# Kernel tuning notes

Measured on AMD Instinct MI355X. Metric: run time of the kernel, lower is better.

Reference implementation:

```python
import jax, jax.numpy as jnp
import numpy as np

NEG_SLOPE = 0.2
BN_EPS = 1e-5


def setup_inputs() -> dict:
    key = jax.random.key(0)
    ks = jax.random.split(key, 12)
    N, E, F_IN, H, C, G, LAT = 50000, 1600000, 128, 2, 64, 512, 32
    x = jax.random.normal(ks[0], (N, F_IN), dtype=jnp.float32)
    edge_index = jax.random.randint(ks[1], (2, E), 0, N, dtype=jnp.int64)
    batch = jnp.sort(jax.random.randint(ks[2], (N,), 0, G, dtype=jnp.int64))
    # GATConv params (PyG layout): lin is Linear(F_IN, H*C, bias=False)
    lin_w = jax.random.normal(ks[3], (H * C, F_IN), dtype=jnp.float32) / np.sqrt(F_IN)
    att_src = jax.random.normal(ks[4], (1, H, C), dtype=jnp.float32) / np.sqrt(C)
    att_dst = jax.random.normal(ks[5], (1, H, C), dtype=jnp.float32) / np.sqrt(C)
    bias = jnp.zeros((H * C,), dtype=jnp.float32)
    bn_gamma = jnp.ones((H * C,), dtype=jnp.float32)
    bn_beta = jnp.zeros((H * C,), dtype=jnp.float32)
    fc_w = jax.random.normal(ks[6], (LAT, H * C), dtype=jnp.float32) / np.sqrt(H * C)
    fc_b = jnp.zeros((LAT,), dtype=jnp.float32)
    return {"x": x, "edge_index": edge_index, "batch": batch, "num_graphs": G,
            "lin_w": lin_w, "att_src": att_src, "att_dst": att_dst, "bias": bias,
            "bn_gamma": bn_gamma, "bn_beta": bn_beta, "fc_w": fc_w, "fc_b": fc_b}


def _gat_conv(x, src, dst, lin_w, att_src, att_dst, bias):
    N = x.shape[0]
    H, C = att_src.shape[1], att_src.shape[2]
    h = (x @ lin_w.T).reshape(N, H, C)                     # [N,H,C]
    a_src = (h * att_src).sum(-1)                          # [N,H]
    a_dst = (h * att_dst).sum(-1)                          # [N,H]
    e = a_src[src] + a_dst[dst]                            # [E,H]
    e = jnp.where(e > 0, e, NEG_SLOPE * e)                 # leaky_relu(0.2)
    # segment softmax over incoming edges of each dst node
    m = jax.ops.segment_max(e, dst, num_segments=N)        # [N,H]
    p = jnp.exp(e - m[dst])
    s = jax.ops.segment_sum(p, dst, num_segments=N)        # [N,H]
    alpha = p / s[dst]                                     # [E,H]
    msg = h[src] * alpha[:, :, None]                       # [E,H,C]
    out = jax.ops.segment_sum(msg, dst, num_segments=N)    # [N,H,C]
    return out.reshape(N, H * C) + bias


def reference(x, edge_index, batch, num_graphs, lin_w, att_src, att_dst, bias,
              bn_gamma, bn_beta, fc_w, fc_b):
    N = x.shape[0]
    loops = jnp.arange(N, dtype=edge_index.dtype)
    src = jnp.concatenate([edge_index[0], loops])          # add_self_loops=True
    dst = jnp.concatenate([edge_index[1], loops])
    h = _gat_conv(x, src, dst, lin_w, att_src, att_dst, bias)
    pooled = jax.ops.segment_sum(h, batch, num_segments=num_graphs)  # [G, H*C]
    mu = pooled.mean(0)
    var = pooled.var(0)
    out = (pooled - mu) / jnp.sqrt(var + BN_EPS) * bn_gamma + bn_beta
    return out @ fc_w.T + fc_b
```

## Files before the change

kernel.cpp:

```cpp
#include <hip/hip_runtime.h>
#include <hip/hip_bf16.h>


#define BKT_SHIFT 8
#define BKT_MASK  255
#define BKT_CAP   14336
#define BIN_TILE  4096

typedef __attribute__((ext_vector_type(8))) short bf16x8;
typedef __attribute__((ext_vector_type(4))) float f32x4;

static __device__ __forceinline__ float lo16(unsigned int u) {
    union { unsigned int i; float f; } c; c.i = u << 16; return c.f;
}
static __device__ __forceinline__ float hi16(unsigned int u) {
    union { unsigned int i; float f; } c; c.i = u & 0xffff0000u; return c.f;
}
static __device__ __forceinline__ unsigned short f2bf(float f) {
    unsigned int b = __builtin_bit_cast(unsigned int, f);
    return (unsigned short)((b >> 16) + ((b >> 15) & 1));
}
static __device__ __forceinline__ float rlane_f(float x, int l) {
    return __builtin_bit_cast(float, __builtin_amdgcn_readlane(__builtin_bit_cast(int, x), l));
}

__global__ __launch_bounds__(256) void k_histprep(const int* __restrict__ ei, int E,
                                                  int* __restrict__ blkhist, int NB,
                                                  const float* __restrict__ w,
                                                  unsigned short* __restrict__ wb,
                                                  float* __restrict__ pooled,
                                                  long long npool, int nbin) {
    const int t = threadIdx.x;
    const int bid = blockIdx.x;
    if (bid < nbin) {
        __shared__ int cnt[1024];
        for (int i = t; i < 1024; i += 256) cnt[i] = 0;
        __syncthreads();
        int base = bid * BIN_TILE;
        int end = min(base + BIN_TILE, E);
        for (int i = base + t; i < end; i += 256)
            atomicAdd(&cnt[ei[E + i] >> BKT_SHIFT], 1);
        __syncthreads();
        int* row = blkhist + (size_t)bid * NB;
        for (int b = t; b < NB; b += 256) row[b] = cnt[b];
    } else if (bid < nbin + 64) {
        int i = (bid - nbin) * 256 + t;
        wb[i] = f2bf(w[i]);
    } else {
        long long i = (long long)(bid - nbin - 64) * 256 + t;
        for (; i < npool; i += 64 * 256) pooled[i] = 0.f;
    }
}

__global__ __launch_bounds__(256) void k_linscan(const float* __restrict__ x,
                                                 const unsigned short* __restrict__ wb,
                                                 const float* __restrict__ att_s,
                                                 const float* __restrict__ att_d,
                                                 unsigned short* __restrict__ h2,
                                                 float* __restrict__ asrc,
                                                 float* __restrict__ adst, int N,
                                                 int* __restrict__ blkhist,
                                                 int* __restrict__ tot,
                                                 int NB, int nbin, int nlin) {
    const int t = threadIdx.x;
    if ((int)blockIdx.x >= nlin) {
        int b = (blockIdx.x - nlin) * 4 + (t >> 6);
        int lane = t & 63;
        if (b >= NB) return;
        int run = 0;
        for (int blk0 = 0; blk0 < nbin; blk0 += 64) {
            int idx = blk0 + lane;
            int v = (idx < nbin) ? blkhist[(size_t)idx * NB + b] : 0;
            int inc = v;
#pragma unroll
            for (int off = 1; off < 64; off <<= 1) {
                int u = __shfl_up(inc, off);
                if (lane >= off) inc += u;
            }
            if (idx < nbin) blkhist[(size_t)idx * NB + b] = run + (inc - v);
            run += __shfl(inc, 63);
        }
        if (lane == 0) tot[b] = run;
        return;
    }
    const int lane = t & 63;
    const int wid = t >> 6;
    const int row0 = (blockIdx.x * 4 + wid) * 16;
    const int rlo = lane & 15;
    const int khi = lane >> 4;

    int arow = row0 + rlo; if (arow >= N) arow = N - 1;
    const float* xrow = x + (long long)arow * 128;
    bf16x8 afrag[4];
#pragma unroll
    for (int ks = 0; ks < 4; ++ks) {
        int k0 = ks * 32 + khi * 8;
        float4 xa = *(const float4*)(xrow + k0);
        float4 xb = *(const float4*)(xrow + k0 + 4);
        bf16x8 a;
        a[0] = (short)f2bf(xa.x); a[1] = (short)f2bf(xa.y);
        a[2] = (short)f2bf(xa.z); a[3] = (short)f2bf(xa.w);
        a[4] = (short)f2bf(xb.x); a[5] = (short)f2bf(xb.y);
        a[6] = (short)f2bf(xb.z); a[7] = (short)f2bf(xb.w);
        afrag[ks] = a;
    }

    float ps0[4] = {0.f,0.f,0.f,0.f}, pd0[4] = {0.f,0.f,0.f,0.f};
    float ps1[4] = {0.f,0.f,0.f,0.f}, pd1[4] = {0.f,0.f,0.f,0.f};

    for (int ct = 0; ct < 8; ++ct) {
        const int col = ct * 16 + rlo;
        f32x4 acc = {0.f, 0.f, 0.f, 0.f};
#pragma unroll
        for (int ks = 0; ks < 4; ++ks) {
            bf16x8 b = *(const bf16x8*)(wb + (size_t)col * 128 + ks * 32 + khi * 8);
            acc = __builtin_amdgcn_mfma_f32_16x16x32_bf16(afrag[ks], b, acc, 0, 0, 0);
        }
        const float as = att_s[col], ad = att_d[col];
        const bool head0 = (ct < 4);
#pragma unroll
        for (int r = 0; r < 4; ++r) {
            int row = row0 + khi * 4 + r;
            if (row < N) h2[(long long)row * 128 + col] = f2bf(acc[r]);
            float v = acc[r];
            if (head0) { ps0[r] = fmaf(v, as, ps0[r]); pd0[r] = fmaf(v, ad, pd0[r]); }
            else       { ps1[r] = fmaf(v, as, ps1[r]); pd1[r] = fmaf(v, ad, pd1[r]); }
        }
    }

#pragma unroll
    for (int off = 1; off <= 8; off <<= 1) {
#pragma unroll
        for (int r = 0; r < 4; ++r) {
            ps0[r] += __shfl_xor(ps0[r], off);
            pd0[r] += __shfl_xor(pd0[r], off);
            ps1[r] += __shfl_xor(ps1[r], off);
            pd1[r] += __shfl_xor(pd1[r], off);
        }
    }
    if (rlo == 0) {
#pragma unroll
        for (int r = 0; r < 4; ++r) {
            int row = row0 + khi * 4 + r;
            if (row < N) {
                asrc[row * 2]     = ps0[r];
                asrc[row * 2 + 1] = ps1[r];
                adst[row * 2]     = pd0[r];
                adst[row * 2 + 1] = pd1[r];
            }
        }
    }
}

__global__ __launch_bounds__(256) void k_bin(const int* __restrict__ ei, int E,
                                             const int* __restrict__ blkhist,
                                             const int* __restrict__ tot,
                                             unsigned int* __restrict__ stage, int NB) {
    __shared__ int gb[1024];
    __shared__ int cnt[1024];
    __shared__ int part[256];
    int t = threadIdx.x;
    const int* row = blkhist + (size_t)blockIdx.x * NB;
    int vals[4]; int s0 = 0;
#pragma unroll
    for (int k = 0; k < 4; ++k) {
        int b2 = t * 4 + k;
        vals[k] = (b2 < NB) ? tot[b2] : 0;
        s0 += vals[k];
    }
    part[t] = s0;
    __syncthreads();
    for (int off = 1; off < 256; off <<= 1) {
        int u = (t >= off) ? part[t - off] : 0;
        __syncthreads();
        part[t] += u;
        __syncthreads();
    }
    int base = part[t] - s0;
#pragma unroll
    for (int k = 0; k < 4; ++k) {
        int b2 = t * 4 + k;
        if (b2 < NB) { gb[b2] = base + row[b2]; cnt[b2] = 0; }
        base += vals[k];
    }
    __syncthreads();
    int ebase = blockIdx.x * BIN_TILE;
    int eend = min(ebase + BIN_TILE, E);
    for (int i = ebase + t; i < eend; i += 256) {
        int s = ei[i];
        int d = ei[E + i];
        int b = d >> BKT_SHIFT;
        int off = atomicAdd(&cnt[b], 1);
        stage[gb[b] + off] = ((unsigned int)(d & BKT_MASK) << 24) | (unsigned int)s;
    }
}

__global__ __launch_bounds__(256) void k_bsort(const int* __restrict__ tot,
                                               const unsigned int* __restrict__ stage,
                                               int* __restrict__ rowptr,
                                               int* __restrict__ csr,
                                               int N, int E, int NB) {
    __shared__ int hist[256];
    __shared__ int sc[256];
    __shared__ int rp[256];
    __shared__ int lc[256];
    __shared__ int part[256];
    __shared__ int s_bb, s_be;
    __shared__ int lout[BKT_CAP];
    int b = blockIdx.x;
    int node0 = b << BKT_SHIFT;
    int nloc = min(256, N - node0);
    int t = threadIdx.x;

    int vals[4]; int s0 = 0;
#pragma unroll
    for (int k = 0; k < 4; ++k) {
        int b2 = t * 4 + k;
        vals[k] = (b2 < NB) ? tot[b2] : 0;
        s0 += vals[k];
    }
    part[t] = s0;
    __syncthreads();
    for (int off = 1; off < 256; off <<= 1) {
        int u = (t >= off) ? part[t - off] : 0;
        __syncthreads();
        part[t] += u;
        __syncthreads();
    }
    int base = part[t] - s0;
#pragma unroll
    for (int k = 0; k < 4; ++k) {
        int b2 = t * 4 + k;
        if (b2 == b) { s_bb = base; s_be = base + vals[k]; }
        base += vals[k];
    }
    __syncthreads();
    const int bb = s_bb, be = s_be;

    hist[t] = 0; lc[t] = 0;
    __syncthreads();
    for (int i = bb + t; i < be; i += 256)
        atomicAdd(&hist[stage[i] >> 24], 1);
    __syncthreads();
    sc[t] = hist[t];
    __syncthreads();
    for (int off = 1; off < 256; off <<= 1) {
        int u = (t >= off) ? sc[t - off] : 0;
        __syncthreads();
        sc[t] += u;
        __syncthreads();
    }
    int rpg = bb + sc[t] - hist[t];
    rp[t] = rpg;
    if (t < nloc) rowptr[node0 + t] = rpg;
    if (b == 0 && t == 0) rowptr[N] = E;
    __syncthreads();
    for (int i = bb + t; i < be; i += 256) {
        unsigned int wrec = stage[i];
        int dl = (int)(wrec >> 24);
        int src = (int)(wrec & 0x00FFFFFFu);
        int pos = rp[dl] + atomicAdd(&lc[dl], 1);
        int rel = pos - bb;
        if (rel < BKT_CAP) lout[rel] = src;
        else csr[pos] = src;
    }
    __syncthreads();
    int cntb = be - bb; if (cntb > BKT_CAP) cntb = BKT_CAP;
    for (int i = t; i < cntb; i += 256) csr[bb + i] = lout[i];
}

__global__ __launch_bounds__(256) void k_agg(const int* __restrict__ rowptr,
                                             const int* __restrict__ csr_src,
                                             const unsigned short* __restrict__ h2,
                                             const float* __restrict__ asrc,
                                             const float* __restrict__ adst,
                                             const float* __restrict__ bias,
                                             const int* __restrict__ batch,
                                             float* __restrict__ pooled, int N) {
    int n = __builtin_amdgcn_readfirstlane(blockIdx.x * 4 + (threadIdx.x >> 6));
    const int lane = threadIdx.x & 63;
    if (n >= N) return;
    const bool lo = (lane < 32);
    const int el = lane & 31;

    float2 adn = *(const float2*)(adst + (size_t)n * 2);
    float2 asn = *(const float2*)(asrc + (size_t)n * 2);
    float e0 = asn.x + adn.x; e0 = e0 > 0.f ? e0 : 0.2f * e0;
    float e1 = asn.y + adn.y; e1 = e1 > 0.f ? e1 : 0.2f * e1;
    float w0 = __expf(e0), w1 = __expf(e1);

    unsigned int v = ((const unsigned int*)(h2 + (size_t)n * 128))[lane];
    float wh = lo ? w0 : w1;
    float aX = wh * lo16(v), aY = wh * hi16(v);
    float ps = 0.f;
    const float adh = lo ? adn.x : adn.y;

    const int beg = rowptr[n], end = rowptr[n + 1];
    for (int base = beg; base < end; base += 32) {
        int cnt = min(32, end - base);
        int sv = n;
        if (el < cnt) sv = csr_src[base + el];
        float av = asrc[(size_t)sv * 2 + (lo ? 0 : 1)];
        float f = av + adh; f = f > 0.f ? f : 0.2f * f;
        float usel = (el < cnt) ? __expf(f) : 0.f;
        ps += usel;

        int k = 0;
        for (; k + 8 <= cnt; k += 8) {
#pragma unroll
            for (int j = 0; j < 8; ++j) {
                int e = k + j;
                int se = __builtin_amdgcn_readlane(sv, e);
                float su0 = rlane_f(usel, e);
                float su1 = rlane_f(usel, e + 32);
                float uu = lo ? su0 : su1;
                unsigned int vv = ((const unsigned int*)(h2 + (size_t)se * 128))[lane];
                aX = fmaf(uu, lo16(vv), aX);
                aY = fmaf(uu, hi16(vv), aY);
            }
        }
        for (; k < cnt; ++k) {
            int se = __builtin_amdgcn_readlane(sv, k);
            float su0 = rlane_f(usel, k);
            float su1 = rlane_f(usel, k + 32);
            float uu = lo ? su0 : su1;
            unsigned int vv = ((const unsigned int*)(h2 + (size_t)se * 128))[lane];
            aX = fmaf(uu, lo16(vv), aX);
            aY = fmaf(uu, hi16(vv), aY);
        }
    }

#pragma unroll
    for (int off = 1; off <= 16; off <<= 1)
        ps += __shfl_xor(ps, off);
    float sdiv = ps + (lo ? w0 : w1);

    int j0 = lane * 2;
    float2 bv = *(const float2*)(bias + j0);
    float o0 = aX / sdiv + bv.x;
    float o1 = aY / sdiv + bv.y;
    int g = batch[n];
    atomicAdd(&pooled[(size_t)g * 128 + j0], o0);
    atomicAdd(&pooled[(size_t)g * 128 + j0 + 1], o1);
}

__global__ __launch_bounds__(512) void k_bnstat(const float* __restrict__ pooled,
                                                const float* __restrict__ gamma,
                                                const float* __restrict__ beta,
                                                float* __restrict__ scale,
                                                float* __restrict__ shift, int G) {
    __shared__ float ls[512], lq[512];
    int t = threadIdx.x;
    int j = t & 127, q = t >> 7;
    int per = G >> 2;
    float sum = 0.f, sq = 0.f;
    for (int g = q * per; g < (q + 1) * per; ++g) {
        float v = pooled[g * 128 + j];
        sum += v; sq += v * v;
    }
    ls[t] = sum; lq[t] = sq;
    __syncthreads();
    if (t < 128) {
        sum = ls[t] + ls[t + 128] + ls[t + 256] + ls[t + 384];
        sq  = lq[t] + lq[t + 128] + lq[t + 256] + lq[t + 384];
        float mu = sum / (float)G;
        float var = sq / (float)G - mu * mu;
        float sc = gamma[t] * rsqrtf(var + 1e-5f);
        scale[t] = sc;
        shift[t] = beta[t] - mu * sc;
    }
}

__global__ __launch_bounds__(128) void k_fc(const float* __restrict__ pooled,
                                            const float* __restrict__ scale,
                                            const float* __restrict__ shift,
                                            const float* __restrict__ fcw,
                                            const float* __restrict__ fcb,
                                            float* __restrict__ out, int LAT) {
    __shared__ float nrm[128];
    int g = blockIdx.x;
    int t = threadIdx.x;
    nrm[t] = pooled[g * 128 + t] * scale[t] + shift[t];
    __syncthreads();
    if (t < LAT) {
        float acc = fcb[t];
#pragma unroll 8
        for (int j = 0; j < 128; ++j)
            acc = fmaf(nrm[j], fcw[t * 128 + j], acc);
        out[g * LAT + t] = acc;
    }
}

extern "C" void kernel_launch(void* const* d_in, const int* in_sizes, int n_in,
                              void* d_out, int out_size, void* d_ws, size_t ws_size,
                              hipStream_t stream) {
    const float* x     = (const float*)d_in[0];
    const int*   ei    = (const int*)d_in[1];
    const int*   batch = (const int*)d_in[2];
    const float* lin_w = (const float*)d_in[4];
    const float* att_s = (const float*)d_in[5];
    const float* att_d = (const float*)d_in[6];
    const float* bias  = (const float*)d_in[7];
    const float* gamma = (const float*)d_in[8];
    const float* beta  = (const float*)d_in[9];
    const float* fcw   = (const float*)d_in[10];
    const float* fcb   = (const float*)d_in[11];
    float* out = (float*)d_out;

    const int N   = in_sizes[2];
    const int E   = in_sizes[1] / 2;
    const int LAT = in_sizes[11];
    const int G   = out_size / LAT;
    const int NB  = (N + 255) >> BKT_SHIFT;
    const int nbin = (E + BIN_TILE - 1) / BIN_TILE;
    const int nlin = (N + 63) / 64;

    char* ws = (char*)d_ws;
    unsigned short* h2 = (unsigned short*)ws; ws += (size_t)N * 128 * 2;
    unsigned short* wb = (unsigned short*)ws; ws += (size_t)128 * 128 * 2;
    float* asrc   = (float*)ws; ws += (size_t)N * 2 * 4;
    float* adst   = (float*)ws; ws += (size_t)N * 2 * 4;
    float* pooled = (float*)ws; ws += (size_t)G * 128 * 4;
    float* scale  = (float*)ws; ws += 128 * 4;
    float* shift  = (float*)ws; ws += 128 * 4;
    int*   tot    = (int*)ws;   ws += (size_t)NB * 4;
    int*   blkhist= (int*)ws;   ws += (size_t)nbin * NB * 4;
    int*   rowptr = (int*)ws;   ws += (size_t)(N + 1) * 4;
    unsigned int* stage = (unsigned int*)ws; ws += (size_t)E * 4;
    int*   csr    = (int*)ws;   ws += (size_t)E * 4;

    k_histprep<<<nbin + 128, 256, 0, stream>>>(ei, E, blkhist, NB, lin_w, wb,
                                               pooled, (long long)G * 128, nbin);
    k_linscan<<<nlin + (NB + 3) / 4, 256, 0, stream>>>(x, wb, att_s, att_d, h2,
                                                       asrc, adst, N, blkhist, tot,
                                                       NB, nbin, nlin);
    k_bin<<<nbin, 256, 0, stream>>>(ei, E, blkhist, tot, stage, NB);
    k_bsort<<<NB, 256, 0, stream>>>(tot, stage, rowptr, csr, N, E, NB);
    k_agg<<<(N + 3) / 4, 256, 0, stream>>>(rowptr, csr, h2, asrc, adst, bias, batch, pooled, N);
    k_bnstat<<<1, 512, 0, stream>>>(pooled, gamma, beta, scale, shift, G);
    k_fc<<<G, 128, 0, stream>>>(pooled, scale, shift, fcw, fcb, out, LAT);
}
```

Before: 179.6 us.

## Fuse CSR build phases into one cooperative kernel and merge BN stats into FC

The histogram, per-bucket scan, edge binning and bucket sort now run as phases of one persistent cooperative kernel separated by grid-wide syncs, instead of four separate launches. The linear projection moves into its own kernel. Batch-norm statistics are recomputed inside each FC block, which removes the single-block stats kernel and the scale/shift buffers. This cuts launch gaps and serialization between small kernels. In exchange it adds grid-sync cost, duplicates the stats reduction across all G blocks, and no longer overlaps the projection with the scan.

After: 327.5 us. +82.4%, slower.

```diff
diff --git a/kernel.cpp b/kernel.cpp
--- a/kernel.cpp
+++ b/kernel.cpp
@@ -1,5 +1,8 @@
 #include <hip/hip_runtime.h>
 #include <hip/hip_bf16.h>
+#include <hip/hip_cooperative_groups.h>
+
+namespace cg = cooperative_groups;
 
 
 #define BKT_SHIFT 8
@@ -24,65 +27,186 @@
     return __builtin_bit_cast(float, __builtin_amdgcn_readlane(__builtin_bit_cast(int, x), l));
 }
 
-__global__ __launch_bounds__(256) void k_histprep(const int* __restrict__ ei, int E,
-                                                  int* __restrict__ blkhist, int NB,
-                                                  const float* __restrict__ w,
-                                                  unsigned short* __restrict__ wb,
-                                                  float* __restrict__ pooled,
-                                                  long long npool, int nbin) {
+__global__ __launch_bounds__(256) void k_csr(const int* __restrict__ ei, int E,
+                                             int* __restrict__ blkhist, int NB,
+                                             const float* __restrict__ w,
+                                             unsigned short* __restrict__ wb,
+                                             float* __restrict__ pooled,
+                                             long long npool, int nbin,
+                                             int* __restrict__ tot,
+                                             int* __restrict__ rowptr,
+                                             int* __restrict__ csr,
+                                             unsigned int* __restrict__ stage,
+                                             int N) {
+    __shared__ int smem[15618];
+    cg::grid_group grid = cg::this_grid();
     const int t = threadIdx.x;
-    const int bid = blockIdx.x;
-    if (bid < nbin) {
-        __shared__ int cnt[1024];
-        for (int i = t; i < 1024; i += 256) cnt[i] = 0;
-        __syncthreads();
-        int base = bid * BIN_TILE;
-        int end = min(base + BIN_TILE, E);
-        for (int i = base + t; i < end; i += 256)
-            atomicAdd(&cnt[ei[E + i] >> BKT_SHIFT], 1);
-        __syncthreads();
-        int* row = blkhist + (size_t)bid * NB;
-        for (int b = t; b < NB; b += 256) row[b] = cnt[b];
-    } else if (bid < nbin + 64) {
-        int i = (bid - nbin) * 256 + t;
-        wb[i] = f2bf(w[i]);
-    } else {
-        long long i = (long long)(bid - nbin - 64) * 256 + t;
-        for (; i < npool; i += 64 * 256) pooled[i] = 0.f;
-    }
-}
-
-__global__ __launch_bounds__(256) void k_linscan(const float* __restrict__ x,
-                                                 const unsigned short* __restrict__ wb,
-                                                 const float* __restrict__ att_s,
-                                                 const float* __restrict__ att_d,
-                                                 unsigned short* __restrict__ h2,
-                                                 float* __restrict__ asrc,
-                                                 float* __restrict__ adst, int N,
-                                                 int* __restrict__ blkhist,
-                                                 int* __restrict__ tot,
-                                                 int NB, int nbin, int nlin) {
+    const int nblk = gridDim.x;
+
+    for (int vb = blockIdx.x; vb < nbin + 128; vb += nblk) {
+        if (vb < nbin) {
+            int* cnt = smem;
+            for (int i = t; i < 1024; i += 256) cnt[i] = 0;
+            __syncthreads();
+            int base = vb * BIN_TILE;
+            int end = min(base + BIN_TILE, E);
+            for (int i = base + t; i < end; i += 256)
+                atomicAdd(&cnt[ei[E + i] >> BKT_SHIFT], 1);
+            __syncthreads();
+            int* row = blkhist + (size_t)vb * NB;
+            for (int b = t; b < NB; b += 256) row[b] = cnt[b];
+            __syncthreads();
+        } else if (vb < nbin + 64) {
+            int i = (vb - nbin) * 256 + t;
+            wb[i] = f2bf(w[i]);
+        } else {
+            long long i = (long long)(vb - nbin - 64) * 256 + t;
+            for (; i < npool; i += 64 * 256) pooled[i] = 0.f;
+        }
+    }
+    grid.sync();
+
+    for (int vb = blockIdx.x; vb < (NB + 3) / 4; vb += nblk) {
+        int b = vb * 4 + (t >> 6);
+        int lane = t & 63;
+        if (b < NB) {
+            int run = 0;
+            for (int blk0 = 0; blk0 < nbin; blk0 += 64) {
+                int idx = blk0 + lane;
+                int v = (idx < nbin) ? blkhist[(size_t)idx * NB + b] : 0;
+                int inc = v;
+#pragma unroll
+                for (int off = 1; off < 64; off <<= 1) {
+                    int u = __shfl_up(inc, off);
+                    if (lane >= off) inc += u;
+                }
+                if (idx < nbin) blkhist[(size_t)idx * NB + b] = run + (inc - v);
+                run += __shfl(inc, 63);
+            }
+            if (lane == 0) tot[b] = run;
+        }
+    }
+    grid.sync();
+
+    for (int vb = blockIdx.x; vb < nbin; vb += nblk) {
+        int* gb   = smem;
+        int* cnt  = smem + 1024;
+        int* part = smem + 2048;
+        const int* row = blkhist + (size_t)vb * NB;
+        int vals[4]; int s0 = 0;
+#pragma unroll
+        for (int k = 0; k < 4; ++k) {
+            int b2 = t * 4 + k;
+            vals[k] = (b2 < NB) ? tot[b2] : 0;
+            s0 += vals[k];
+        }
+        part[t] = s0;
+        __syncthreads();
+        for (int off = 1; off < 256; off <<= 1) {
+            int u = (t >= off) ? part[t - off] : 0;
+            __syncthreads();
+            part[t] += u;
+            __syncthreads();
+        }
+        int base = part[t] - s0;
+#pragma unroll
+        for (int k = 0; k < 4; ++k) {
+            int b2 = t * 4 + k;
+            if (b2 < NB) { gb[b2] = base + row[b2]; cnt[b2] = 0; }
+            base += vals[k];
+        }
+        __syncthreads();
+        int ebase = vb * BIN_TILE;
+        int eend = min(ebase + BIN_TILE, E);
+        for (int i = ebase + t; i < eend; i += 256) {
+            int s = ei[i];
+            int d = ei[E + i];
+            int b = d >> BKT_SHIFT;
+            int off = atomicAdd(&cnt[b], 1);
+            stage[gb[b] + off] = ((unsigned int)(d & BKT_MASK) << 24) | (unsigned int)s;
+        }
+        __syncthreads();
+    }
+    grid.sync();
+
+    for (int vb = blockIdx.x; vb < NB; vb += nblk) {
+        int* lout = smem;
+        int* hist = smem + 14336;
+        int* sc   = smem + 14592;
+        int* rp   = smem + 14848;
+        int* lc   = smem + 15104;
+        int* part = smem + 15360;
+        int* sbb  = smem + 15616;
+        int node0 = vb << BKT_SHIFT;
+        int nloc = min(256, N - node0);
+
+        int vals[4]; int s0 = 0;
+#pragma unroll
+        for (int k = 0; k < 4; ++k) {
+            int b2 = t * 4 + k;
+            vals[k] = (b2 < NB) ? tot[b2] : 0;
+            s0 += vals[k];
+        }
+        part[t] = s0;
+        __syncthreads();
+        for (int off = 1; off < 256; off <<= 1) {
+            int u = (t >= off) ? part[t - off] : 0;
+            __syncthreads();
+            part[t] += u;
+            __syncthreads();
+        }
+        int base = part[t] - s0;
+#pragma unroll
+        for (int k = 0; k < 4; ++k) {
+            int b2 = t * 4 + k;
+            if (b2 == vb) { sbb[0] = base; sbb[1] = base + vals[k]; }
+            base += vals[k];
+        }
+        __syncthreads();
+        const int bb = sbb[0], be = sbb[1];
+
+        hist[t] = 0; lc[t] = 0;
+        __syncthreads();
+        for (int i = bb + t; i < be; i += 256)
+            atomicAdd(&hist[stage[i] >> 24], 1);
+        __syncthreads();
+        sc[t] = hist[t];
+        __syncthreads();
+        for (int off = 1; off < 256; off <<= 1) {
+            int u = (t >= off) ? sc[t - off] : 0;
+            __syncthreads();
+            sc[t] += u;
+            __syncthreads();
+        }
+        int rpg = bb + sc[t] - hist[t];
+        rp[t] = rpg;
+        if (t < nloc) rowptr[node0 + t] = rpg;
+        if (vb == 0 && t == 0) rowptr[N] = E;
+        __syncthreads();
+        for (int i = bb + t; i < be; i += 256) {
+            unsigned int wrec = stage[i];
+            int dl = (int)(wrec >> 24);
+            int src = (int)(wrec & 0x00FFFFFFu);
+            int pos = rp[dl] + atomicAdd(&lc[dl], 1);
+            int rel = pos - bb;
+            if (rel < BKT_CAP) lout[rel] = src;
+            else csr[pos] = src;
+        }
+        __syncthreads();
+        int cntb = be - bb; if (cntb > BKT_CAP) cntb = BKT_CAP;
+        for (int i = t; i < cntb; i += 256) csr[bb + i] = lout[i];
+        __syncthreads();
+    }
+}
+
+__global__ __launch_bounds__(256) void k_lin(const float* __restrict__ x,
+                                             const unsigned short* __restrict__ wb,
+                                             const float* __restrict__ att_s,
+                                             const float* __restrict__ att_d,
+                                             unsigned short* __restrict__ h2,
+                                             float* __restrict__ asrc,
+                                             float* __restrict__ adst, int N) {
     const int t = threadIdx.x;
-    if ((int)blockIdx.x >= nlin) {
-        int b = (blockIdx.x - nlin) * 4 + (t >> 6);
-        int lane = t & 63;
-        if (b >= NB) return;
-        int run = 0;
-        for (int blk0 = 0; blk0 < nbin; blk0 += 64) {
-            int idx = blk0 + lane;
-            int v = (idx < nbin) ? blkhist[(size_t)idx * NB + b] : 0;
-            int inc = v;
-#pragma unroll
-            for (int off = 1; off < 64; off <<= 1) {
-                int u = __shfl_up(inc, off);
-                if (lane >= off) inc += u;
-            }
-            if (idx < nbin) blkhist[(size_t)idx * NB + b] = run + (inc - v);
-            run += __shfl(inc, 63);
-        }
-        if (lane == 0) tot[b] = run;
-        return;
-    }
     const int lane = t & 63;
     const int wid = t >> 6;
     const int row0 = (blockIdx.x * 4 + wid) * 16;
@@ -150,123 +274,6 @@
             }
         }
     }
-}
-
-__global__ __launch_bounds__(256) void k_bin(const int* __restrict__ ei, int E,
-                                             const int* __restrict__ blkhist,
-                                             const int* __restrict__ tot,
-                                             unsigned int* __restrict__ stage, int NB) {
-    __shared__ int gb[1024];
-    __shared__ int cnt[1024];
-    __shared__ int part[256];
-    int t = threadIdx.x;
-    const int* row = blkhist + (size_t)blockIdx.x * NB;
-    int vals[4]; int s0 = 0;
-#pragma unroll
-    for (int k = 0; k < 4; ++k) {
-        int b2 = t * 4 + k;
-        vals[k] = (b2 < NB) ? tot[b2] : 0;
-        s0 += vals[k];
-    }
-    part[t] = s0;
-    __syncthreads();
-    for (int off = 1; off < 256; off <<= 1) {
-        int u = (t >= off) ? part[t - off] : 0;
-        __syncthreads();
-        part[t] += u;
-        __syncthreads();
-    }
-    int base = part[t] - s0;
-#pragma unroll
-    for (int k = 0; k < 4; ++k) {
-        int b2 = t * 4 + k;
-        if (b2 < NB) { gb[b2] = base + row[b2]; cnt[b2] = 0; }
-        base += vals[k];
-    }
-    __syncthreads();
-    int ebase = blockIdx.x * BIN_TILE;
-    int eend = min(ebase + BIN_TILE, E);
-    for (int i = ebase + t; i < eend; i += 256) {
-        int s = ei[i];
-        int d = ei[E + i];
-        int b = d >> BKT_SHIFT;
-        int off = atomicAdd(&cnt[b], 1);
-        stage[gb[b] + off] = ((unsigned int)(d & BKT_MASK) << 24) | (unsigned int)s;
-    }
-}
-
-__global__ __launch_bounds__(256) void k_bsort(const int* __restrict__ tot,
-                                               const unsigned int* __restrict__ stage,
-                                               int* __restrict__ rowptr,
-                                               int* __restrict__ csr,
-                                               int N, int E, int NB) {
-    __shared__ int hist[256];
-    __shared__ int sc[256];
-    __shared__ int rp[256];
-    __shared__ int lc[256];
-    __shared__ int part[256];
-    __shared__ int s_bb, s_be;
-    __shared__ int lout[BKT_CAP];
-    int b = blockIdx.x;
-    int node0 = b << BKT_SHIFT;
-    int nloc = min(256, N - node0);
-    int t = threadIdx.x;
-
-    int vals[4]; int s0 = 0;
-#pragma unroll
-    for (int k = 0; k < 4; ++k) {
-        int b2 = t * 4 + k;
-        vals[k] = (b2 < NB) ? tot[b2] : 0;
-        s0 += vals[k];
-    }
-    part[t] = s0;
-    __syncthreads();
-    for (int off = 1; off < 256; off <<= 1) {
-        int u = (t >= off) ? part[t - off] : 0;
-        __syncthreads();
-        part[t] += u;
-        __syncthreads();
-    }
-    int base = part[t] - s0;
-#pragma unroll
-    for (int k = 0; k < 4; ++k) {
-        int b2 = t * 4 + k;
-        if (b2 == b) { s_bb = base; s_be = base + vals[k]; }
-        base += vals[k];
-    }
-    __syncthreads();
-    const int bb = s_bb, be = s_be;
-
-    hist[t] = 0; lc[t] = 0;
-    __syncthreads();
-    for (int i = bb + t; i < be; i += 256)
-        atomicAdd(&hist[stage[i] >> 24], 1);
-    __syncthreads();
-    sc[t] = hist[t];
-    __syncthreads();
-    for (int off = 1; off < 256; off <<= 1) {
-        int u = (t >= off) ? sc[t - off] : 0;
-        __syncthreads();
-        sc[t] += u;
-        __syncthreads();
-    }
-    int rpg = bb + sc[t] - hist[t];
-    rp[t] = rpg;
-    if (t < nloc) rowptr[node0 + t] = rpg;
-    if (b == 0 && t == 0) rowptr[N] = E;
-    __syncthreads();
-    for (int i = bb + t; i < be; i += 256) {
-        unsigned int wrec = stage[i];
-        int dl = (int)(wrec >> 24);
-        int src = (int)(wrec & 0x00FFFFFFu);
-        int pos = rp[dl] + atomicAdd(&lc[dl], 1);
-        int rel = pos - bb;
-        if (rel < BKT_CAP) lout[rel] = src;
-        else csr[pos] = src;
-    }
-    __syncthreads();
-    int cntb = be - bb; if (cntb > BKT_CAP) cntb = BKT_CAP;
-    for (int i = t; i < cntb; i += 256) csr[bb + i] = lout[i];
 }
 
 __global__ __launch_bounds__(256) void k_agg(const int* __restrict__ rowptr,
@@ -344,43 +351,27 @@
     atomicAdd(&pooled[(size_t)g * 128 + j0 + 1], o1);
 }
 
-__global__ __launch_bounds__(512) void k_bnstat(const float* __restrict__ pooled,
+__global__ __launch_bounds__(128) void k_fcstat(const float* __restrict__ pooled,
                                                 const float* __restrict__ gamma,
                                                 const float* __restrict__ beta,
-                                                float* __restrict__ scale,
-                                                float* __restrict__ shift, int G) {
-    __shared__ float ls[512], lq[512];
+                                                const float* __restrict__ fcw,
+                                                const float* __restrict__ fcb,
+                                                float* __restrict__ out, int G, int LAT) {
+    __shared__ float nrm[128];
     int t = threadIdx.x;
-    int j = t & 127, q = t >> 7;
-    int per = G >> 2;
     float sum = 0.f, sq = 0.f;
-    for (int g = q * per; g < (q + 1) * per; ++g) {
-        float v = pooled[g * 128 + j];
+#pragma unroll 8
+    for (int g = 0; g < G; ++g) {
+        float v = pooled[(size_t)g * 128 + t];
         sum += v; sq += v * v;
     }
-    ls[t] = sum; lq[t] = sq;
-    __syncthreads();
-    if (t < 128) {
-        sum = ls[t] + ls[t + 128] + ls[t + 256] + ls[t + 384];
-        sq  = lq[t] + lq[t + 128] + lq[t + 256] + lq[t + 384];
-        float mu = sum / (float)G;
-        float var = sq / (float)G - mu * mu;
-        float sc = gamma[t] * rsqrtf(var + 1e-5f);
-        scale[t] = sc;
-        shift[t] = beta[t] - mu * sc;
-    }
-}
-
-__global__ __launch_bounds__(128) void k_fc(const float* __restrict__ pooled,
-                                            const float* __restrict__ scale,
-                                            const float* __restrict__ shift,
-                                            const float* __restrict__ fcw,
-                                            const float* __restrict__ fcb,
-                                            float* __restrict__ out, int LAT) {
-    __shared__ float nrm[128];
+    float mu = sum / (float)G;
+    float var = sq / (float)G - mu * mu;
+    float sc = gamma[t] * rsqrtf(var + 1e-5f);
+    float sh = beta[t] - mu * sc;
+
     int g = blockIdx.x;
-    int t = threadIdx.x;
-    nrm[t] = pooled[g * 128 + t] * scale[t] + shift[t];
+    nrm[t] = pooled[(size_t)g * 128 + t] * sc + sh;
     __syncthreads();
     if (t < LAT) {
         float acc = fcb[t];
@@ -421,22 +412,24 @@
     float* asrc   = (float*)ws; ws += (size_t)N * 2 * 4;
     float* adst   = (float*)ws; ws += (size_t)N * 2 * 4;
     float* pooled = (float*)ws; ws += (size_t)G * 128 * 4;
-    float* scale  = (float*)ws; ws += 128 * 4;
-    float* shift  = (float*)ws; ws += 128 * 4;
     int*   tot    = (int*)ws;   ws += (size_t)NB * 4;
     int*   blkhist= (int*)ws;   ws += (size_t)nbin * NB * 4;
     int*   rowptr = (int*)ws;   ws += (size_t)(N + 1) * 4;
     unsigned int* stage = (unsigned int*)ws; ws += (size_t)E * 4;
     int*   csr    = (int*)ws;   ws += (size_t)E * 4;
 
-    k_histprep<<<nbin + 128, 256, 0, stream>>>(ei, E, blkhist, NB, lin_w, wb,
-                                               pooled, (long long)G * 128, nbin);
-    k_linscan<<<nlin + (NB + 3) / 4, 256, 0, stream>>>(x, wb, att_s, att_d, h2,
-                                                       asrc, adst, N, blkhist, tot,
-                                                       NB, nbin, nlin);
-    k_bin<<<nbin, 256, 0, stream>>>(ei, E, blkhist, tot, stage, NB);
-    k_bsort<<<NB, 256, 0, stream>>>(tot, stage, rowptr, csr, N, E, NB);
+    long long npool = (long long)G * 128;
+    int E_ = E, NB_ = NB, nbin_ = nbin, N_ = N;
+    void* cargs[] = {
+        (void*)&ei, (void*)&E_, (void*)&blkhist, (void*)&NB_,
+        (void*)&lin_w, (void*)&wb, (void*)&pooled, (void*)&npool,
+        (void*)&nbin_, (void*)&tot, (void*)&rowptr, (void*)&csr,
+        (void*)&stage, (void*)&N_
+    };
+    hipLaunchCooperativeKernel((const void*)k_csr, dim3(nbin), dim3(256),
+                               cargs, 0, stream);
+
+    k_lin<<<nlin, 256, 0, stream>>>(x, wb, att_s, att_d, h2, asrc, adst, N);
     k_agg<<<(N + 3) / 4, 256, 0, stream>>>(rowptr, csr, h2, asrc, adst, bias, batch, pooled, N);
-    k_bnstat<<<1, 512, 0, stream>>>(pooled, gamma, beta, scale, shift, G);
-    k_fc<<<G, 128, 0, stream>>>(pooled, scale, shift, fcw, fcb, out, LAT);
-}
+    k_fcstat<<<G, 128, 0, stream>>>(pooled, gamma, beta, fcw, fcb, out, G, LAT);
+}
```
